# Optimization experiments

Measured on AMD Instinct MI355X. Metric: run time of the kernel, lower is better.

The kernel has to match this reference:

```python
import jax, jax.numpy as jnp
import numpy as np

N = 10000
E = 160000
NEG_SLOPE = 0.2
BN_EPS = 1e-5


def _gat_conv(x, W, a_src, a_dst, b, src, dst, n, heads):
    # PyG GATConv, concat=False (mean over heads), shared lin for src/dst.
    H = heads
    C = W.shape[1] // H
    h = (x @ W).reshape(n, H, C)                       # (N,H,C)
    e_s = jnp.einsum('nhc,hc->nh', h, a_src)           # (N,H)
    e_d = jnp.einsum('nhc,hc->nh', h, a_dst)
    alpha = jax.nn.leaky_relu(e_s[src] + e_d[dst], NEG_SLOPE)   # (E',H)
    amax = jax.ops.segment_max(alpha, dst, num_segments=n)       # per-dst softmax
    ex = jnp.exp(alpha - amax[dst])
    denom = jax.ops.segment_sum(ex, dst, num_segments=n)
    w = ex / (denom[dst] + 1e-16)
    out = jax.ops.segment_sum(h[src] * w[:, :, None], dst, num_segments=n)  # (N,H,C)
    return out.mean(axis=1) + b


def _bn(x, g, b):
    mu = x.mean(axis=0)
    var = x.var(axis=0)  # biased, as torch BN training forward
    return (x - mu) * jax.lax.rsqrt(var + BN_EPS) * g + b


def setup_inputs() -> dict:
    key = jax.random.key(0)
    ks = jax.random.split(key, 32)
    d = {}
    d['x'] = jax.random.normal(ks[0], (N, 64), jnp.float32)
    d['edge_index'] = jax.random.randint(ks[1], (2, E), 0, N, jnp.int64)
    s = lambda k, shape, fan: jax.random.normal(k, shape, jnp.float32) * (1.0 / np.sqrt(fan))
    d['Wp'] = s(ks[2], (64, 128), 64); d['bp'] = jnp.zeros((128,), jnp.float32)
    # conv0: 8 heads, per-head 128
    d['W0'] = s(ks[3], (128, 8 * 128), 128); d['as0'] = s(ks[4], (8, 128), 128)
    d['ad0'] = s(ks[5], (8, 128), 128); d['b0'] = jnp.zeros((128,), jnp.float32)
    d['g0'] = jnp.ones((128,), jnp.float32); d['be0'] = jnp.zeros((128,), jnp.float32)
    # conv1: same shape
    d['W1'] = s(ks[6], (128, 8 * 128), 128); d['as1'] = s(ks[7], (8, 128), 128)
    d['ad1'] = s(ks[8], (8, 128), 128); d['b1'] = jnp.zeros((128,), jnp.float32)
    d['g1'] = jnp.ones((128,), jnp.float32); d['be1'] = jnp.zeros((128,), jnp.float32)
    # conv2: 1 head, out 64
    d['W2'] = s(ks[9], (128, 64), 128); d['as2'] = s(ks[10], (1, 64), 64)
    d['ad2'] = s(ks[11], (1, 64), 64); d['b2'] = jnp.zeros((64,), jnp.float32)
    d['g2'] = jnp.ones((64,), jnp.float32); d['be2'] = jnp.zeros((64,), jnp.float32)
    # residual projection for layer 2 (128 -> 64)
    d['Wr'] = s(ks[12], (128, 64), 128); d['br'] = jnp.zeros((64,), jnp.float32)
    return d


def reference(x, edge_index, Wp, bp, W0, as0, ad0, b0, g0, be0,
              W1, as1, ad1, b1, g1, be1, W2, as2, ad2, b2, g2, be2, Wr, br):
    n = x.shape[0]
    loops = jnp.arange(n, dtype=edge_index.dtype)
    src = jnp.concatenate([edge_index[0], loops])  # add_self_loops=True
    dst = jnp.concatenate([edge_index[1], loops])
    h = x @ Wp + bp
    # layer 0 (8 heads, identity residual)
    hr = h
    h = jax.nn.elu(_bn(_gat_conv(h, W0, as0, ad0, b0, src, dst, n, 8), g0, be0)) + hr
    # layer 1
    hr = h
    h = jax.nn.elu(_bn(_gat_conv(h, W1, as1, ad1, b1, src, dst, n, 8), g1, be1)) + hr
    # layer 2 (1 head, linear residual 128->64)
    hr = h @ Wr + br
    h = jax.nn.elu(_bn(_gat_conv(h, W2, as2, ad2, b2, src, dst, n, 1), g2, be2)) + hr
    return h
```

## Files before the change

kernel.cpp:

```cpp
#include <hip/hip_runtime.h>
#include <hip/hip_bf16.h>
#include <cstdint>
#include <cstddef>

#define TPB 256

typedef __attribute__((ext_vector_type(8))) short bf16x8;
typedef __attribute__((ext_vector_type(4))) float f32x4;

static __device__ __forceinline__ float bf2f(unsigned short u) {
  union { unsigned int i; float f; } c;
  c.i = ((unsigned int)u) << 16;
  return c.f;
}

__global__ void detect_kernel(const unsigned int* __restrict__ w, int* __restrict__ flag) {
  __shared__ int any32;
  if (threadIdx.x == 0) any32 = 0;
  __syncthreads();
  for (int i = threadIdx.x; i < 1024; i += TPB)
    if (w[2 * i + 1] != 0u) any32 = 1;
  __syncthreads();
  if (threadIdx.x == 0) *flag = any32;
}

__global__ void decode_kernel(const void* __restrict__ raw, const int* __restrict__ flag,
                              int* __restrict__ src, int* __restrict__ dst, int E, int n) {
  int i = blockIdx.x * TPB + threadIdx.x;
  int tot = E + n;
  if (i >= tot) return;
  if (i < E) {
    if (*flag) {
      const int* p = (const int*)raw;
      src[i] = p[i];
      dst[i] = p[E + i];
    } else {
      const long long* p = (const long long*)raw;
      src[i] = (int)p[i];
      dst[i] = (int)p[E + i];
    }
  } else {
    src[i] = i - E;
    dst[i] = i - E;
  }
}

__global__ void count_kernel(const int* __restrict__ dst, int* __restrict__ counts, int etot) {
  int i = blockIdx.x * TPB + threadIdx.x;
  if (i < etot) atomicAdd(&counts[dst[i]], 1);
}

__global__ void scan_kernel(const int* __restrict__ counts, int* __restrict__ row_ptr, int n) {
  __shared__ int part[TPB];
  int tid = threadIdx.x;
  int chunk = (n + TPB - 1) / TPB;
  int begin = tid * chunk;
  int end = begin + chunk; if (end > n) end = n;
  int s = 0;
  for (int i = begin; i < end && i < n; i++) s += counts[i];
  part[tid] = s;
  __syncthreads();
  for (int off = 1; off < TPB; off <<= 1) {
    int v = (tid >= off) ? part[tid - off] : 0;
    __syncthreads();
    part[tid] += v;
    __syncthreads();
  }
  int base = (tid == 0) ? 0 : part[tid - 1];
  for (int i = begin; i < end && i < n; i++) { row_ptr[i] = base; base += counts[i]; }
  if (tid == TPB - 1) row_ptr[n] = base;
}

__global__ void fill_kernel(const int* __restrict__ src, const int* __restrict__ dst,
                            const int* __restrict__ row_ptr, int* __restrict__ fill,
                            int* __restrict__ sorted_src, int etot) {
  int i = blockIdx.x * TPB + threadIdx.x;
  if (i >= etot) return;
  int d = dst[i];
  int pos = row_ptr[d] + atomicAdd(&fill[d], 1);
  sorted_src[pos] = src[i];
}

__global__ void f32_to_bf16_kernel(const float* __restrict__ in, __hip_bfloat16* __restrict__ out, int n) {
  int i = blockIdx.x * TPB + threadIdx.x;
  if (i < n) out[i] = __float2bfloat16(in[i]);
}

__global__ void f32_to_bf16_T_kernel(const float* __restrict__ in, __hip_bfloat16* __restrict__ out,
                                     int K, int N) {
  __shared__ float tile[32][33];
  const int k0 = blockIdx.x * 32, n0 = blockIdx.y * 32;
  const int tx = threadIdx.x & 31, ty = threadIdx.x >> 5;
  for (int r = ty; r < 32; r += 8) {
    int k = k0 + r, n = n0 + tx;
    tile[r][tx] = (k < K && n < N) ? in[(size_t)k * N + n] : 0.f;
  }
  __syncthreads();
  for (int r = ty; r < 32; r += 8) {
    int n = n0 + r, k = k0 + tx;
    if (n < N && k < K) out[(size_t)n * K + k] = __float2bfloat16(tile[tx][r]);
  }
}

__global__ __launch_bounds__(256) void gemm_bf16t_kernel(
    const short* __restrict__ A, const short* __restrict__ Bt,
    const float* __restrict__ bias, float* __restrict__ C,
    __hip_bfloat16* __restrict__ Cb, int M, int Ncols, int K,
    const float* __restrict__ asrc, const float* __restrict__ adst,
    float* __restrict__ es_out, float* __restrict__ ed_out, int H, int hshift) {
  __shared__ short As[64][40];
  __shared__ short Bs[128][40];

  const int tid = threadIdx.x;
  const int lane = tid & 63;
  const int w = tid >> 6;
  const int bm = blockIdx.x * 64;
  const int bn = blockIdx.y * 128;

  f32x4 acc[8];
#pragma unroll
  for (int nt = 0; nt < 8; nt++) acc[nt] = (f32x4){0.f, 0.f, 0.f, 0.f};

  const int arow = tid >> 2;
  const int akk = (tid & 3) << 3;
  const int brow = tid >> 1;
  const int bkk = (tid & 1) << 4;

  for (int k0 = 0; k0 < K; k0 += 32) {
    {
      int gr = bm + arow;
      if (gr < M) {
        *(bf16x8*)&As[arow][akk] = *(const bf16x8*)&A[(size_t)gr * K + k0 + akk];
      } else {
        bf16x8 z = {0, 0, 0, 0, 0, 0, 0, 0};
        *(bf16x8*)&As[arow][akk] = z;
      }
    }
    {
      int gbn = bn + brow;
      if (gbn < Ncols) {
        const short* bp = &Bt[(size_t)gbn * K + k0 + bkk];
        *(bf16x8*)&Bs[brow][bkk]     = *(const bf16x8*)bp;
        *(bf16x8*)&Bs[brow][bkk + 8] = *(const bf16x8*)(bp + 8);
      } else {
        bf16x8 z = {0, 0, 0, 0, 0, 0, 0, 0};
        *(bf16x8*)&Bs[brow][bkk] = z;
        *(bf16x8*)&Bs[brow][bkk + 8] = z;
      }
    }
    __syncthreads();

    bf16x8 a = *(const bf16x8*)&As[w * 16 + (lane & 15)][(lane >> 4) * 8];
#pragma unroll
    for (int nt = 0; nt < 8; nt++) {
      bf16x8 b = *(const bf16x8*)&Bs[nt * 16 + (lane & 15)][(lane >> 4) * 8];
      acc[nt] = __builtin_amdgcn_mfma_f32_16x16x32_bf16(a, b, acc[nt], 0, 0, 0);
    }
    __syncthreads();
  }

  float p1[4] = {0.f, 0.f, 0.f, 0.f};
  float p2[4] = {0.f, 0.f, 0.f, 0.f};

#pragma unroll
  for (int nt = 0; nt < 8; nt++) {
    int gc = bn + nt * 16 + (lane & 15);
    if (gc >= Ncols) continue;
    float bv = bias ? bias[gc] : 0.f;
    float asv = es_out ? asrc[gc] : 0.f;
    float adv = es_out ? adst[gc] : 0.f;
#pragma unroll
    for (int q = 0; q < 4; q++) {
      int gr = bm + w * 16 + (lane >> 4) * 4 + q;
      if (gr < M) {
        float val = acc[nt][q] + bv;
        if (C) C[(size_t)gr * Ncols + gc] = val;
        if (Cb) Cb[(size_t)gr * Ncols + gc] = __float2bfloat16(val);
        p1[q] += val * asv;
        p2[q] += val * adv;
      }
    }
  }

  if (es_out) {
    const int head = bn >> hshift;
#pragma unroll
    for (int q = 0; q < 4; q++) {
      float s1 = p1[q], s2 = p2[q];
      s1 += __shfl_xor(s1, 1); s2 += __shfl_xor(s2, 1);
      s1 += __shfl_xor(s1, 2); s2 += __shfl_xor(s2, 2);
      s1 += __shfl_xor(s1, 4); s2 += __shfl_xor(s2, 4);
      s1 += __shfl_xor(s1, 8); s2 += __shfl_xor(s2, 8);
      int gr = bm + w * 16 + (lane >> 4) * 4 + q;
      if ((lane & 15) == 0 && gr < M) {
        es_out[(size_t)gr * H + head] = s1;
        ed_out[(size_t)gr * H + head] = s2;
      }
    }
  }
}

__global__ __launch_bounds__(256) void gat_weights_kernel(
    const int* __restrict__ row_ptr, const int* __restrict__ srcs,
    const float* __restrict__ es, const float* __restrict__ ed,
    float* __restrict__ wbuf, int etot, int n) {
  const int wave = threadIdx.x >> 6, lane = threadIdx.x & 63;
  const int v = blockIdx.x * 4 + wave;
  if (v >= n) return;
  const int begin = row_ptr[v], deg = row_ptr[v + 1] - begin;
  const int eh = lane & 7, ee = lane >> 3;
  const float edv = ed[(size_t)v * 8 + eh];

  if (deg <= 64) {
    float a[8];
#pragma unroll
    for (int b = 0; b < 8; b++) {
      a[b] = -1e30f;
      int e = b * 8 + ee;
      if (e < deg) {
        int s = srcs[begin + e];
        float t = es[(size_t)s * 8 + eh] + edv;
        a[b] = t > 0.f ? t : 0.2f * t;
      }
    }
    float m = a[0];
#pragma unroll
    for (int b = 1; b < 8; b++) m = fmaxf(m, a[b]);
    m = fmaxf(m, __shfl_xor(m, 8));
    m = fmaxf(m, __shfl_xor(m, 16));
    m = fmaxf(m, __shfl_xor(m, 32));
    float dsum = 0.f;
#pragma unroll
    for (int b = 0; b < 8; b++) { a[b] = __expf(a[b] - m); dsum += a[b]; }
    dsum += __shfl_xor(dsum, 8);
    dsum += __shfl_xor(dsum, 16);
    dsum += __shfl_xor(dsum, 32);
    const float invd = 1.0f / (dsum + 1e-16f);
#pragma unroll
    for (int b = 0; b < 8; b++) {
      int e = b * 8 + ee;
      if (e < deg) wbuf[(size_t)eh * etot + begin + e] = a[b] * invd;
    }
  } else {
    float m = -1e30f;
    for (int e = ee; e < deg; e += 8) {
      int s = srcs[begin + e];
      float t = es[(size_t)s * 8 + eh] + edv;
      t = t > 0.f ? t : 0.2f * t;
      m = fmaxf(m, t);
    }
    m = fmaxf(m, __shfl_xor(m, 8));
    m = fmaxf(m, __shfl_xor(m, 16));
    m = fmaxf(m, __shfl_xor(m, 32));
    float dsum = 0.f;
    for (int e = ee; e < deg; e += 8) {
      int s = srcs[begin + e];
      float t = es[(size_t)s * 8 + eh] + edv;
      t = t > 0.f ? t : 0.2f * t;
      dsum += __expf(t - m);
    }
    dsum += __shfl_xor(dsum, 8);
    dsum += __shfl_xor(dsum, 16);
    dsum += __shfl_xor(dsum, 32);
    const float invd = 1.0f / (dsum + 1e-16f);
    for (int e = ee; e < deg; e += 8) {
      int s = srcs[begin + e];
      float t = es[(size_t)s * 8 + eh] + edv;
      t = t > 0.f ? t : 0.2f * t;
      wbuf[(size_t)eh * etot + begin + e] = __expf(t - m) * invd;
    }
  }
}

__global__ __launch_bounds__(256) void gat_gather_head_kernel(
    const int* __restrict__ row_ptr, const int* __restrict__ srcs,
    const unsigned short* __restrict__ gb, const float* __restrict__ wbuf,
    unsigned short* __restrict__ partial, int etot, int n, int nb) {
  const int h = blockIdx.x & 7;
  const int nblk = blockIdx.x >> 3;
  const int wave = threadIdx.x >> 6, lane = threadIdx.x & 63;
  const int per = (n + nb - 1) / nb;
  const int v1 = min((nblk + 1) * per, n);
  const float* wb = wbuf + (size_t)h * etot;
  const unsigned short* gsl = gb + h * 128;
  unsigned short* pout = partial + (size_t)h * n * 128;
  const int c = lane * 2;

  for (int v = nblk * per + wave; v < v1; v += 4) {
    const int begin = row_ptr[v];
    const int deg = row_ptr[v + 1] - begin;
    float ax = 0.f, ay = 0.f;
    for (int base = 0; base < deg; base += 64) {
      const int cnt = min(64, deg - base);
      int sv = 0; float wv = 0.f;
      if (lane < cnt) {
        sv = srcs[begin + base + lane];
        wv = wb[begin + base + lane];
      }
      for (int j0 = 0; j0 < cnt; j0 += 8) {
        int s0 = __shfl(sv, j0 + 0), s1 = __shfl(sv, j0 + 1);
        int s2 = __shfl(sv, j0 + 2), s3 = __shfl(sv, j0 + 3);
        int s4 = __shfl(sv, j0 + 4), s5 = __shfl(sv, j0 + 5);
        int s6 = __shfl(sv, j0 + 6), s7 = __shfl(sv, j0 + 7);
        float w0 = __shfl(wv, j0 + 0), w1 = __shfl(wv, j0 + 1);
        float w2 = __shfl(wv, j0 + 2), w3 = __shfl(wv, j0 + 3);
        float w4 = __shfl(wv, j0 + 4), w5 = __shfl(wv, j0 + 5);
        float w6 = __shfl(wv, j0 + 6), w7 = __shfl(wv, j0 + 7);
        unsigned int u0 = *(const unsigned int*)&gsl[(size_t)s0 * 1024 + c];
        unsigned int u1 = *(const unsigned int*)&gsl[(size_t)s1 * 1024 + c];
        unsigned int u2 = *(const unsigned int*)&gsl[(size_t)s2 * 1024 + c];
        unsigned int u3 = *(const unsigned int*)&gsl[(size_t)s3 * 1024 + c];
        unsigned int u4 = *(const unsigned int*)&gsl[(size_t)s4 * 1024 + c];
        unsigned int u5 = *(const unsigned int*)&gsl[(size_t)s5 * 1024 + c];
        unsigned int u6 = *(const unsigned int*)&gsl[(size_t)s6 * 1024 + c];
        unsigned int u7 = *(const unsigned int*)&gsl[(size_t)s7 * 1024 + c];
        ax += w0 * bf2f((unsigned short)u0) + w1 * bf2f((unsigned short)u1)
            + w2 * bf2f((unsigned short)u2) + w3 * bf2f((unsigned short)u3)
            + w4 * bf2f((unsigned short)u4) + w5 * bf2f((unsigned short)u5)
            + w6 * bf2f((unsigned short)u6) + w7 * bf2f((unsigned short)u7);
        ay += w0 * bf2f((unsigned short)(u0 >> 16)) + w1 * bf2f((unsigned short)(u1 >> 16))
            + w2 * bf2f((unsigned short)(u2 >> 16)) + w3 * bf2f((unsigned short)(u3 >> 16))
            + w4 * bf2f((unsigned short)(u4 >> 16)) + w5 * bf2f((unsigned short)(u5 >> 16))
            + w6 * bf2f((unsigned short)(u6 >> 16)) + w7 * bf2f((unsigned short)(u7 >> 16));
      }
    }
    __hip_bfloat16 bx = __float2bfloat16(ax), by = __float2bfloat16(ay);
    unsigned int o = (unsigned int)*(unsigned short*)&bx
                   | ((unsigned int)*(unsigned short*)&by << 16);
    *(unsigned int*)&pout[(size_t)v * 128 + c] = o;
  }
}

__global__ void gat_reduce_kernel(const unsigned short* __restrict__ partial,
                                  const float* __restrict__ bias,
                                  float* __restrict__ out, int n) {
  int idx = blockIdx.x * TPB + threadIdx.x;
  if (idx >= n * 64) return;
  int v = idx >> 6, c = (idx & 63) * 2;
  float sx = 0.f, sy = 0.f;
#pragma unroll
  for (int h = 0; h < 8; h++) {
    unsigned int u = *(const unsigned int*)&partial[(size_t)h * n * 128 + (size_t)v * 128 + c];
    sx += bf2f((unsigned short)u);
    sy += bf2f((unsigned short)(u >> 16));
  }
  out[(size_t)v * 128 + c]     = sx * 0.125f + bias[c];
  out[(size_t)v * 128 + c + 1] = sy * 0.125f + bias[c + 1];
}

__global__ __launch_bounds__(256) void gat_aggregate1_kernel(
    const int* __restrict__ row_ptr, const int* __restrict__ srcs,
    const float* __restrict__ g, const float* __restrict__ es,
    const float* __restrict__ ed, const float* __restrict__ bias,
    float* __restrict__ out, int n) {
  const int wave = threadIdx.x >> 6;
  const int lane = threadIdx.x & 63;
  const int v = blockIdx.x * 4 + wave;

  __shared__ float wlds[4][64];
  __shared__ int slds[4][64];

  if (v >= n) return;

  const int begin = row_ptr[v];
  const int deg = row_ptr[v + 1] - begin;
  const float edv = ed[v];

  float acc = 0.f;

  if (deg <= 64) {
    float a = -1e30f;
    int s = 0;
    if (lane < deg) {
      s = srcs[begin + lane];
      float t = es[s] + edv;
      a = t > 0.f ? t : 0.2f * t;
    }
    float m = a;
#pragma unroll
    for (int off = 32; off > 0; off >>= 1) m = fmaxf(m, __shfl_xor(m, off));
    float p = __expf(a - m);
    float dsum = p;
#pragma unroll
    for (int off = 32; off > 0; off >>= 1) dsum += __shfl_xor(dsum, off);
    const float invd = 1.0f / (dsum + 1e-16f);
    wlds[wave][lane] = p * invd;
    slds[wave][lane] = s;

    const int npad = (deg + 7) & ~7;
    for (int j0 = 0; j0 < npad; j0 += 8) {
      float w0 = wlds[wave][j0 + 0], w1 = wlds[wave][j0 + 1];
      float w2 = wlds[wave][j0 + 2], w3 = wlds[wave][j0 + 3];
      float w4 = wlds[wave][j0 + 4], w5 = wlds[wave][j0 + 5];
      float w6 = wlds[wave][j0 + 6], w7 = wlds[wave][j0 + 7];
      int s0 = slds[wave][j0 + 0], s1 = slds[wave][j0 + 1];
      int s2 = slds[wave][j0 + 2], s3 = slds[wave][j0 + 3];
      int s4 = slds[wave][j0 + 4], s5 = slds[wave][j0 + 5];
      int s6 = slds[wave][j0 + 6], s7 = slds[wave][j0 + 7];
      float f0 = g[(size_t)s0 * 64 + lane];
      float f1 = g[(size_t)s1 * 64 + lane];
      float f2 = g[(size_t)s2 * 64 + lane];
      float f3 = g[(size_t)s3 * 64 + lane];
      float f4 = g[(size_t)s4 * 64 + lane];
      float f5 = g[(size_t)s5 * 64 + lane];
      float f6 = g[(size_t)s6 * 64 + lane];
      float f7 = g[(size_t)s7 * 64 + lane];
      acc += (w0 * f0 + w1 * f1) + (w2 * f2 + w3 * f3)
           + (w4 * f4 + w5 * f5) + (w6 * f6 + w7 * f7);
    }
  } else {
    float pm = -1e30f;
    for (int j = lane; j < deg; j += 64) {
      float a = es[srcs[begin + j]] + edv;
      a = a > 0.f ? a : 0.2f * a;
      pm = fmaxf(pm, a);
    }
#pragma unroll
    for (int off = 32; off > 0; off >>= 1) pm = fmaxf(pm, __shfl_xor(pm, off));
    float ps = 0.f;
    for (int j = lane; j < deg; j += 64) {
      float a = es[srcs[begin + j]] + edv;
      a = a > 0.f ? a : 0.2f * a;
      ps += __expf(a - pm);
    }
#pragma unroll
    for (int off = 32; off > 0; off >>= 1) ps += __shfl_xor(ps, off);
    const float invd = 1.0f / (ps + 1e-16f);

    for (int base = 0; base < deg; base += 64) {
      int cnt = min(64, deg - base);
      float wv = 0.f; int s = 0;
      if (lane < cnt) {
        s = srcs[begin + base + lane];
        float a = es[s] + edv;
        a = a > 0.f ? a : 0.2f * a;
        wv = __expf(a - pm) * invd;
      }
      wlds[wave][lane] = wv;
      slds[wave][lane] = s;
      const int npad = (cnt + 7) & ~7;
      for (int j0 = 0; j0 < npad; j0 += 8) {
        float w0 = wlds[wave][j0 + 0], w1 = wlds[wave][j0 + 1];
        float w2 = wlds[wave][j0 + 2], w3 = wlds[wave][j0 + 3];
        float w4 = wlds[wave][j0 + 4], w5 = wlds[wave][j0 + 5];
        float w6 = wlds[wave][j0 + 6], w7 = wlds[wave][j0 + 7];
        int s0 = slds[wave][j0 + 0], s1 = slds[wave][j0 + 1];
        int s2 = slds[wave][j0 + 2], s3 = slds[wave][j0 + 3];
        int s4 = slds[wave][j0 + 4], s5 = slds[wave][j0 + 5];
        int s6 = slds[wave][j0 + 6], s7 = slds[wave][j0 + 7];
        float f0 = g[(size_t)s0 * 64 + lane];
        float f1 = g[(size_t)s1 * 64 + lane];
        float f2 = g[(size_t)s2 * 64 + lane];
        float f3 = g[(size_t)s3 * 64 + lane];
        float f4 = g[(size_t)s4 * 64 + lane];
        float f5 = g[(size_t)s5 * 64 + lane];
        float f6 = g[(size_t)s6 * 64 + lane];
        float f7 = g[(size_t)s7 * 64 + lane];
        acc += (w0 * f0 + w1 * f1) + (w2 * f2 + w3 * f3)
             + (w4 * f4 + w5 * f5) + (w6 * f6 + w7 * f7);
      }
    }
  }
  out[(size_t)v * 64 + lane] = acc + bias[lane];
}

template <int C>
__global__ void bn_stats_kernel(const float* __restrict__ x, int n, float* __restrict__ sums) {
  constexpr int T = 256;
  constexpr int RPI = T / C;
  constexpr int ITER = 8;
  constexpr int ROWS = RPI * ITER;
  int c = threadIdx.x % C;
  int r0 = threadIdx.x / C;
  int rowBase = blockIdx.x * ROWS;
  float s = 0.f, q = 0.f;
  for (int it = 0; it < ITER; ++it) {
    int r = rowBase + it * RPI + r0;
    if (r < n) {
      float v = x[(size_t)r * C + c];
      s += v; q += v * v;
    }
  }
  __shared__ float ls[T], lq[T];
  ls[threadIdx.x] = s; lq[threadIdx.x] = q;
  __syncthreads();
  if (threadIdx.x < C) {
    float ts = 0.f, tq = 0.f;
    for (int r = 0; r < RPI; ++r) { ts += ls[c + r * C]; tq += lq[c + r * C]; }
    atomicAdd(&sums[c], ts);
    atomicAdd(&sums[C + c], tq);
  }
}

template <int C>
__global__ void bn_elu_res_kernel(const float* __restrict__ x, const float* __restrict__ sums,
                                  const float* __restrict__ gamma, const float* __restrict__ beta,
                                  const float* __restrict__ res, float* __restrict__ out,
                                  __hip_bfloat16* __restrict__ outb, int n) {
  int i = blockIdx.x * TPB + threadIdx.x;
  if (i >= n * C) return;
  int c = i % C;
  float inv_n = 1.0f / (float)n;
  float mu = sums[c] * inv_n;
  float var = sums[C + c] * inv_n - mu * mu;
  float y = (x[i] - mu) * rsqrtf(var + 1e-5f) * gamma[c] + beta[c];
  y = y > 0.f ? y : expm1f(y);
  y += res[i];
  out[i] = y;
  if (outb) outb[i] = __float2bfloat16(y);
}

extern "C" void kernel_launch(void* const* d_in, const int* in_sizes, int n_in,
                              void* d_out, int out_size, void* d_ws, size_t ws_size,
                              hipStream_t stream) {
  const float* x   = (const float*)d_in[0];
  const void*  ei  = d_in[1];
  const float* Wp  = (const float*)d_in[2];
  const float* bp  = (const float*)d_in[3];
  const float* W0  = (const float*)d_in[4];
  const float* as0 = (const float*)d_in[5];
  const float* ad0 = (const float*)d_in[6];
  const float* b0  = (const float*)d_in[7];
  const float* g0  = (const float*)d_in[8];
  const float* be0 = (const float*)d_in[9];
  const float* W1  = (const float*)d_in[10];
  const float* as1 = (const float*)d_in[11];
  const float* ad1 = (const float*)d_in[12];
  const float* b1  = (const float*)d_in[13];
  const float* g1  = (const float*)d_in[14];
  const float* be1 = (const float*)d_in[15];
  const float* W2  = (const float*)d_in[16];
  const float* as2 = (const float*)d_in[17];
  const float* ad2 = (const float*)d_in[18];
  const float* b2  = (const float*)d_in[19];
  const float* g2  = (const float*)d_in[20];
  const float* be2 = (const float*)d_in[21];
  const float* Wr  = (const float*)d_in[22];
  const float* br  = (const float*)d_in[23];

  const int N = in_sizes[0] / 64;
  const int E = in_sizes[1] / 2;
  const int ETOT = E + N;

  char* wsp = (char*)d_ws;
  size_t off = 0;
  auto alloc = [&](size_t bytes) -> void* {
    void* p = wsp + off;
    off += (bytes + 255) & ~(size_t)255;
    return p;
  };
  int*   flag    = (int*)alloc(4);
  int*   e_src   = (int*)alloc((size_t)ETOT * 4);
  int*   e_dst   = (int*)alloc((size_t)ETOT * 4);
  int*   counts  = (int*)alloc((size_t)N * 4);
  int*   fillc   = (int*)alloc((size_t)N * 4);
  int*   row_ptr = (int*)alloc((size_t)(N + 1) * 4);
  int*   s_src   = (int*)alloc((size_t)ETOT * 4);
  float* hA      = (float*)alloc((size_t)N * 128 * 4);
  float* hB      = (float*)alloc((size_t)N * 128 * 4);
  float* gat     = (float*)alloc((size_t)N * 128 * 4);
  float* es      = (float*)alloc((size_t)N * 8 * 4);
  float* ed      = (float*)alloc((size_t)N * 8 * 4);
  float* bnsum   = (float*)alloc(2 * 128 * 4);
  float* wbuf    = (float*)alloc((size_t)ETOT * 8 * 4);
  __hip_bfloat16* gbufb = (__hip_bfloat16*)alloc((size_t)N * 1024 * 2);
  float* gbuf    = (float*)gbufb;
  unsigned short* partial = (unsigned short*)alloc((size_t)N * 1024 * 2);
  __hip_bfloat16* xb  = (__hip_bfloat16*)alloc((size_t)N * 64 * 2);
  __hip_bfloat16* hAb = (__hip_bfloat16*)alloc((size_t)N * 128 * 2);
  __hip_bfloat16* hBb = (__hip_bfloat16*)alloc((size_t)N * 128 * 2);
  __hip_bfloat16* WpT = (__hip_bfloat16*)alloc((size_t)128 * 64 * 2);
  __hip_bfloat16* W0T = (__hip_bfloat16*)alloc((size_t)1024 * 128 * 2);
  __hip_bfloat16* W1T = (__hip_bfloat16*)alloc((size_t)1024 * 128 * 2);
  __hip_bfloat16* W2T = (__hip_bfloat16*)alloc((size_t)64 * 128 * 2);
  __hip_bfloat16* WrT = (__hip_bfloat16*)alloc((size_t)64 * 128 * 2);

  const int egrid = (ETOT + TPB - 1) / TPB;
  const int mgrid = (N + 63) / 64;
  const int NB = 512;
  auto cgrid = [](int n) { return (n + TPB - 1) / TPB; };

  detect_kernel<<<1, TPB, 0, stream>>>((const unsigned int*)ei, flag);
  decode_kernel<<<egrid, TPB, 0, stream>>>(ei, flag, e_src, e_dst, E, N);
  hipMemsetAsync(counts, 0, (size_t)N * 4, stream);
  hipMemsetAsync(fillc, 0, (size_t)N * 4, stream);
  count_kernel<<<egrid, TPB, 0, stream>>>(e_dst, counts, ETOT);
  scan_kernel<<<1, TPB, 0, stream>>>(counts, row_ptr, N);
  fill_kernel<<<egrid, TPB, 0, stream>>>(e_src, e_dst, row_ptr, fillc, s_src, ETOT);

  f32_to_bf16_kernel<<<cgrid(N * 64), TPB, 0, stream>>>(x, xb, N * 64);
  f32_to_bf16_T_kernel<<<dim3(2, 4), 256, 0, stream>>>(Wp, WpT, 64, 128);
  f32_to_bf16_T_kernel<<<dim3(4, 32), 256, 0, stream>>>(W0, W0T, 128, 1024);
  f32_to_bf16_T_kernel<<<dim3(4, 32), 256, 0, stream>>>(W1, W1T, 128, 1024);
  f32_to_bf16_T_kernel<<<dim3(4, 2), 256, 0, stream>>>(W2, W2T, 128, 64);
  f32_to_bf16_T_kernel<<<dim3(4, 2), 256, 0, stream>>>(Wr, WrT, 128, 64);

  gemm_bf16t_kernel<<<dim3(mgrid, 1), 256, 0, stream>>>(
      (const short*)xb, (const short*)WpT, bp, hA, hAb, N, 128, 64,
      nullptr, nullptr, nullptr, nullptr, 1, 7);

  gemm_bf16t_kernel<<<dim3(mgrid, 8), 256, 0, stream>>>(
      (const short*)hAb, (const short*)W0T, nullptr, nullptr, gbufb, N, 1024, 128,
      as0, ad0, es, ed, 8, 7);
  gat_weights_kernel<<<(N + 3) / 4, 256, 0, stream>>>(row_ptr, s_src, es, ed, wbuf, ETOT, N);
  gat_gather_head_kernel<<<8 * NB, 256, 0, stream>>>(
      row_ptr, s_src, (const unsigned short*)gbufb, wbuf, partial, ETOT, N, NB);
  gat_reduce_kernel<<<cgrid(N * 64), TPB, 0, stream>>>(partial, b0, gat, N);
  hipMemsetAsync(bnsum, 0, 2 * 128 * 4, stream);
  bn_stats_kernel<128><<<(N + 15) / 16, 256, 0, stream>>>(gat, N, bnsum);
  bn_elu_res_kernel<128><<<cgrid(N * 128), TPB, 0, stream>>>(gat, bnsum, g0, be0, hA, hB, hBb, N);

  gemm_bf16t_kernel<<<dim3(mgrid, 8), 256, 0, stream>>>(
      (const short*)hBb, (const short*)W1T, nullptr, nullptr, gbufb, N, 1024, 128,
      as1, ad1, es, ed, 8, 7);
  gat_weights_kernel<<<(N + 3) / 4, 256, 0, stream>>>(row_ptr, s_src, es, ed, wbuf, ETOT, N);
  gat_gather_head_kernel<<<8 * NB, 256, 0, stream>>>(
      row_ptr, s_src, (const unsigned short*)gbufb, wbuf, partial, ETOT, N, NB);
  gat_reduce_kernel<<<cgrid(N * 64), TPB, 0, stream>>>(partial, b1, gat, N);
  hipMemsetAsync(bnsum, 0, 2 * 128 * 4, stream);
  bn_stats_kernel<128><<<(N + 15) / 16, 256, 0, stream>>>(gat, N, bnsum);
  bn_elu_res_kernel<128><<<cgrid(N * 128), TPB, 0, stream>>>(gat, bnsum, g1, be1, hB, hA, hAb, N);

  gemm_bf16t_kernel<<<dim3(mgrid, 1), 256, 0, stream>>>(
      (const short*)hAb, (const short*)WrT, br, hB, nullptr, N, 64, 128,
      nullptr, nullptr, nullptr, nullptr, 1, 7);
  gemm_bf16t_kernel<<<dim3(mgrid, 1), 256, 0, stream>>>(
      (const short*)hAb, (const short*)W2T, nullptr, gbuf, nullptr, N, 64, 128,
      as2, ad2, es, ed, 1, 6);
  gat_aggregate1_kernel<<<(N + 3) / 4, 256, 0, stream>>>(row_ptr, s_src, gbuf, es, ed, b2, gat, N);
  hipMemsetAsync(bnsum, 0, 2 * 64 * 4, stream);
  bn_stats_kernel<64><<<(N + 31) / 32, 256, 0, stream>>>(gat, N, bnsum);
  bn_elu_res_kernel<64><<<cgrid(N * 64), TPB, 0, stream>>>(gat, bnsum, g2, be2, hB, (float*)d_out, nullptr, N);
}
```

Measured before the change: 314.5 us.

## Vectorize per-head gather with 16B loads and fuse head reduce with BN stats

The per-head gather now has each wave split into 4 groups of 16 lanes. Each lane loads 8 bf16 channels with a single 16-byte load, and the 4 groups work on different edges, with source ids and weights staged through LDS instead of shuffles. Partial sums are combined across groups with xor-shuffles. The head-mean reduce kernel is merged with the BN statistics pass using a grid-stride loop and block-level atomics, which removes one kernel launch and one full read of the aggregated output per layer. This adds LDS use and padded iterations that read zeroed slots, and changes the floating-point summation order.

```diff
diff --git a/kernel.cpp b/kernel.cpp
--- a/kernel.cpp
+++ b/kernel.cpp
@@ -6,12 +6,17 @@
 #define TPB 256
 
 typedef __attribute__((ext_vector_type(8))) short bf16x8;
+typedef __attribute__((ext_vector_type(8))) unsigned short ushort8;
 typedef __attribute__((ext_vector_type(4))) float f32x4;
 
 static __device__ __forceinline__ float bf2f(unsigned short u) {
   union { unsigned int i; float f; } c;
   c.i = ((unsigned int)u) << 16;
   return c.f;
+}
+static __device__ __forceinline__ unsigned short f2us(float v) {
+  __hip_bfloat16 b = __float2bfloat16(v);
+  return *(unsigned short*)&b;
 }
 
 __global__ void detect_kernel(const unsigned int* __restrict__ w, int* __restrict__ flag) {
@@ -279,17 +284,25 @@
   const int h = blockIdx.x & 7;
   const int nblk = blockIdx.x >> 3;
   const int wave = threadIdx.x >> 6, lane = threadIdx.x & 63;
+
+  __shared__ float wlds[4][64];
+  __shared__ int slds[4][64];
+
   const int per = (n + nb - 1) / nb;
   const int v1 = min((nblk + 1) * per, n);
   const float* wb = wbuf + (size_t)h * etot;
   const unsigned short* gsl = gb + h * 128;
   unsigned short* pout = partial + (size_t)h * n * 128;
-  const int c = lane * 2;
+  const int g = lane >> 4;
+  const int c8 = (lane & 15) * 8;
 
   for (int v = nblk * per + wave; v < v1; v += 4) {
     const int begin = row_ptr[v];
     const int deg = row_ptr[v + 1] - begin;
-    float ax = 0.f, ay = 0.f;
+    float acc[8];
+#pragma unroll
+    for (int k = 0; k < 8; k++) acc[k] = 0.f;
+
     for (int base = 0; base < deg; base += 64) {
       const int cnt = min(64, deg - base);
       int sv = 0; float wv = 0.f;
@@ -297,55 +310,81 @@
         sv = srcs[begin + base + lane];
         wv = wb[begin + base + lane];
       }
-      for (int j0 = 0; j0 < cnt; j0 += 8) {
-        int s0 = __shfl(sv, j0 + 0), s1 = __shfl(sv, j0 + 1);
-        int s2 = __shfl(sv, j0 + 2), s3 = __shfl(sv, j0 + 3);
-        int s4 = __shfl(sv, j0 + 4), s5 = __shfl(sv, j0 + 5);
-        int s6 = __shfl(sv, j0 + 6), s7 = __shfl(sv, j0 + 7);
-        float w0 = __shfl(wv, j0 + 0), w1 = __shfl(wv, j0 + 1);
-        float w2 = __shfl(wv, j0 + 2), w3 = __shfl(wv, j0 + 3);
-        float w4 = __shfl(wv, j0 + 4), w5 = __shfl(wv, j0 + 5);
-        float w6 = __shfl(wv, j0 + 6), w7 = __shfl(wv, j0 + 7);
-        unsigned int u0 = *(const unsigned int*)&gsl[(size_t)s0 * 1024 + c];
-        unsigned int u1 = *(const unsigned int*)&gsl[(size_t)s1 * 1024 + c];
-        unsigned int u2 = *(const unsigned int*)&gsl[(size_t)s2 * 1024 + c];
-        unsigned int u3 = *(const unsigned int*)&gsl[(size_t)s3 * 1024 + c];
-        unsigned int u4 = *(const unsigned int*)&gsl[(size_t)s4 * 1024 + c];
-        unsigned int u5 = *(const unsigned int*)&gsl[(size_t)s5 * 1024 + c];
-        unsigned int u6 = *(const unsigned int*)&gsl[(size_t)s6 * 1024 + c];
-        unsigned int u7 = *(const unsigned int*)&gsl[(size_t)s7 * 1024 + c];
-        ax += w0 * bf2f((unsigned short)u0) + w1 * bf2f((unsigned short)u1)
-            + w2 * bf2f((unsigned short)u2) + w3 * bf2f((unsigned short)u3)
-            + w4 * bf2f((unsigned short)u4) + w5 * bf2f((unsigned short)u5)
-            + w6 * bf2f((unsigned short)u6) + w7 * bf2f((unsigned short)u7);
-        ay += w0 * bf2f((unsigned short)(u0 >> 16)) + w1 * bf2f((unsigned short)(u1 >> 16))
-            + w2 * bf2f((unsigned short)(u2 >> 16)) + w3 * bf2f((unsigned short)(u3 >> 16))
-            + w4 * bf2f((unsigned short)(u4 >> 16)) + w5 * bf2f((unsigned short)(u5 >> 16))
-            + w6 * bf2f((unsigned short)(u6 >> 16)) + w7 * bf2f((unsigned short)(u7 >> 16));
-      }
-    }
-    __hip_bfloat16 bx = __float2bfloat16(ax), by = __float2bfloat16(ay);
-    unsigned int o = (unsigned int)*(unsigned short*)&bx
-                   | ((unsigned int)*(unsigned short*)&by << 16);
-    *(unsigned int*)&pout[(size_t)v * 128 + c] = o;
-  }
-}
-
-__global__ void gat_reduce_kernel(const unsigned short* __restrict__ partial,
-                                  const float* __restrict__ bias,
-                                  float* __restrict__ out, int n) {
-  int idx = blockIdx.x * TPB + threadIdx.x;
-  if (idx >= n * 64) return;
-  int v = idx >> 6, c = (idx & 63) * 2;
-  float sx = 0.f, sy = 0.f;
-#pragma unroll
-  for (int h = 0; h < 8; h++) {
-    unsigned int u = *(const unsigned int*)&partial[(size_t)h * n * 128 + (size_t)v * 128 + c];
-    sx += bf2f((unsigned short)u);
-    sy += bf2f((unsigned short)(u >> 16));
-  }
-  out[(size_t)v * 128 + c]     = sx * 0.125f + bias[c];
-  out[(size_t)v * 128 + c + 1] = sy * 0.125f + bias[c + 1];
+      slds[wave][lane] = sv;
+      wlds[wave][lane] = wv;
+      const int npad = (cnt + 15) & ~15;
+      for (int j0 = 0; j0 < npad; j0 += 16) {
+        int s0 = slds[wave][j0 + g];
+        int s1 = slds[wave][j0 + 4 + g];
+        int s2 = slds[wave][j0 + 8 + g];
+        int s3 = slds[wave][j0 + 12 + g];
+        float w0 = wlds[wave][j0 + g];
+        float w1 = wlds[wave][j0 + 4 + g];
+        float w2 = wlds[wave][j0 + 8 + g];
+        float w3 = wlds[wave][j0 + 12 + g];
+        ushort8 u0 = *(const ushort8*)&gsl[(size_t)s0 * 1024 + c8];
+        ushort8 u1 = *(const ushort8*)&gsl[(size_t)s1 * 1024 + c8];
+        ushort8 u2 = *(const ushort8*)&gsl[(size_t)s2 * 1024 + c8];
+        ushort8 u3 = *(const ushort8*)&gsl[(size_t)s3 * 1024 + c8];
+#pragma unroll
+        for (int k = 0; k < 8; k++) {
+          acc[k] += w0 * bf2f(u0[k]) + w1 * bf2f(u1[k])
+                  + w2 * bf2f(u2[k]) + w3 * bf2f(u3[k]);
+        }
+      }
+    }
+
+#pragma unroll
+    for (int k = 0; k < 8; k++) {
+      acc[k] += __shfl_xor(acc[k], 16);
+      acc[k] += __shfl_xor(acc[k], 32);
+    }
+    if (lane < 16) {
+      unsigned int o[4];
+#pragma unroll
+      for (int k = 0; k < 4; k++)
+        o[k] = (unsigned int)f2us(acc[2 * k]) | ((unsigned int)f2us(acc[2 * k + 1]) << 16);
+      *(uint4*)&pout[(size_t)v * 128 + c8] = *(uint4*)o;
+    }
+  }
+}
+
+__global__ __launch_bounds__(256) void gat_reduce_bn_kernel(
+    const unsigned short* __restrict__ partial, const float* __restrict__ bias,
+    float* __restrict__ out, float* __restrict__ sums, int n) {
+  const int t = threadIdx.x;
+  const int stride = gridDim.x * TPB;
+  float s0 = 0.f, q0 = 0.f, s1 = 0.f, q1 = 0.f;
+  for (int idx = blockIdx.x * TPB + t; idx < n * 64; idx += stride) {
+    int v = idx >> 6, c = (idx & 63) * 2;
+    float sx = 0.f, sy = 0.f;
+#pragma unroll
+    for (int h = 0; h < 8; h++) {
+      unsigned int u = *(const unsigned int*)&partial[(size_t)h * n * 128 + (size_t)v * 128 + c];
+      sx += bf2f((unsigned short)u);
+      sy += bf2f((unsigned short)(u >> 16));
+    }
+    float x0 = sx * 0.125f + bias[c];
+    float x1 = sy * 0.125f + bias[c + 1];
+    out[(size_t)v * 128 + c]     = x0;
+    out[(size_t)v * 128 + c + 1] = x1;
+    s0 += x0; q0 += x0 * x0;
+    s1 += x1; q1 += x1 * x1;
+  }
+  __shared__ float ls0[TPB], lq0[TPB], ls1[TPB], lq1[TPB];
+  ls0[t] = s0; lq0[t] = q0; ls1[t] = s1; lq1[t] = q1;
+  __syncthreads();
+  if (t < 64) {
+    float S0 = ls0[t] + ls0[t + 64] + ls0[t + 128] + ls0[t + 192];
+    float Q0 = lq0[t] + lq0[t + 64] + lq0[t + 128] + lq0[t + 192];
+    float S1 = ls1[t] + ls1[t + 64] + ls1[t + 128] + ls1[t + 192];
+    float Q1 = lq1[t] + lq1[t + 64] + lq1[t + 128] + lq1[t + 192];
+    int c = t * 2;
+    atomicAdd(&sums[c], S0);
+    atomicAdd(&sums[128 + c], Q0);
+    atomicAdd(&sums[c + 1], S1);
+    atomicAdd(&sums[128 + c + 1], Q1);
+  }
 }
 
 __global__ __launch_bounds__(256) void gat_aggregate1_kernel(
@@ -605,9 +644,8 @@
   gat_weights_kernel<<<(N + 3) / 4, 256, 0, stream>>>(row_ptr, s_src, es, ed, wbuf, ETOT, N);
   gat_gather_head_kernel<<<8 * NB, 256, 0, stream>>>(
       row_ptr, s_src, (const unsigned short*)gbufb, wbuf, partial, ETOT, N, NB);
-  gat_reduce_kernel<<<cgrid(N * 64), TPB, 0, stream>>>(partial, b0, gat, N);
   hipMemsetAsync(bnsum, 0, 2 * 128 * 4, stream);
-  bn_stats_kernel<128><<<(N + 15) / 16, 256, 0, stream>>>(gat, N, bnsum);
+  gat_reduce_bn_kernel<<<512, 256, 0, stream>>>(partial, b0, gat, bnsum, N);
   bn_elu_res_kernel<128><<<cgrid(N * 128), TPB, 0, stream>>>(gat, bnsum, g0, be0, hA, hB, hBb, N);
 
   gemm_bf16t_kernel<<<dim3(mgrid, 8), 256, 0, stream>>>(
@@ -616,9 +654,8 @@
   gat_weights_kernel<<<(N + 3) / 4, 256, 0, stream>>>(row_ptr, s_src, es, ed, wbuf, ETOT, N);
   gat_gather_head_kernel<<<8 * NB, 256, 0, stream>>>(
       row_ptr, s_src, (const unsigned short*)gbufb, wbuf, partial, ETOT, N, NB);
-  gat_reduce_kernel<<<cgrid(N * 64), TPB, 0, stream>>>(partial, b1, gat, N);
   hipMemsetAsync(bnsum, 0, 2 * 128 * 4, stream);
-  bn_stats_kernel<128><<<(N + 15) / 16, 256, 0, stream>>>(gat, N, bnsum);
+  gat_reduce_bn_kernel<<<512, 256, 0, stream>>>(partial, b1, gat, bnsum, N);
   bn_elu_res_kernel<128><<<cgrid(N * 128), TPB, 0, stream>>>(gat, bnsum, g1, be1, hB, hA, hAb, N);
 
   gemm_bf16t_kernel<<<dim3(mgrid, 1), 256, 0, stream>>>(
```

New measurement: 312.4 us. Within noise of the previous version (-0.7%).
